# Kernel tuning notes

Measured on AMD Instinct MI355X. Metric: run time of the kernel, lower is better.

Reference implementation:

```python
import jax, jax.numpy as jnp
import numpy as np

N_Q = 16
N_K = 16
D_QK = 64
D_V = 64
# torch module default scale=1.0 saturates softmax at feature width 1024;
# we use the conventional sqrt(d) scale for well-conditioned numerics.
SCALE = 32.0  # sqrt(N_Q * D_QK)
DROPOUT_P = 0.0  # dropout is identity at p=0


def setup_inputs() -> dict:
    key = jax.random.key(0)
    kq, kk, kv = jax.random.split(key, 3)
    S = 8192
    return {
        "query": jax.random.normal(kq, (S, N_Q, D_QK), dtype=jnp.float32),
        "key": jax.random.normal(kk, (S, N_K, D_QK), dtype=jnp.float32),
        "value": jax.random.normal(kv, (S, N_K, D_V), dtype=jnp.float32),
    }


def reference(query, key, value):
    # Flatten trailing (head, dim) into one feature axis, as the torch view does.
    q = query.reshape(-1, N_Q * D_QK)            # [S_q, 1024]
    k = key.reshape(-1, N_K * D_QK)              # [S_k, 1024]
    v = value.reshape(-1, N_K * D_V)             # [S_k, 1024]
    scores = jnp.matmul(q, k.T) / SCALE          # [S_q, S_k]
    attn = jax.nn.softmax(scores, axis=-1)       # dropout_p=0 -> identity
    out = jnp.matmul(attn, v)                    # [S_q, 1024]
    return out.reshape(query.shape[:-1] + (-1,))  # [S_q, N_Q, D_V]
```

## Files before the change

### kernel.cpp

```cpp
#include <hip/hip_runtime.h>
#include <hip/hip_bf16.h>


typedef __bf16 bf16x8 __attribute__((ext_vector_type(8)));
typedef float f32x4 __attribute__((ext_vector_type(4)));
typedef const __attribute__((address_space(1))) unsigned int* as1p;
typedef __attribute__((address_space(3))) unsigned int* as3p;
typedef unsigned short u16;

__device__ __forceinline__ u16 f2bf(float x) {
  unsigned u = __float_as_uint(x);
  u += 0x7fffu + ((u >> 16) & 1u);
  return (u16)(u >> 16);
}
__device__ __forceinline__ float bf2f(u16 b) { return __uint_as_float(((unsigned)b) << 16); }
__device__ __forceinline__ unsigned pack2(float lo, float hi) {
  return (unsigned)f2bf(lo) | ((unsigned)f2bf(hi) << 16);
}

#define BAR()   do { __builtin_amdgcn_s_barrier(); __builtin_amdgcn_sched_barrier(0); } while (0)
#define LGKM0() do { asm volatile("s_waitcnt lgkmcnt(0)" ::: "memory"); __builtin_amdgcn_sched_barrier(0); } while (0)

__global__ __launch_bounds__(256) void cvt_bf16(const float* __restrict__ in,
                                                unsigned short* __restrict__ out) {
  const size_t i = (size_t)blockIdx.x * 256 + threadIdx.x;
  const float4* p = (const float4*)in + i * 2;
  float4 a = p[0], b = p[1];
  uint4 o;
  o.x = pack2(a.x, a.y);
  o.y = pack2(a.z, a.w);
  o.z = pack2(b.x, b.y);
  o.w = pack2(b.z, b.w);
  ((uint4*)out)[i] = o;
}

__global__ __launch_bounds__(256) void transpose_bf16(const float* __restrict__ V,
                                                      unsigned short* __restrict__ VT) {
  __shared__ float t[64][65];
  const int rb = blockIdx.x * 64;
  const int cb = blockIdx.y * 64;
  const int tid = threadIdx.x;
#pragma unroll
  for (int it = 0; it < 4; ++it) {
    int r = it * 16 + (tid >> 4);
    int c = (tid & 15) * 4;
    float4 x = *(const float4*)(V + (size_t)(rb + r) * 1024 + cb + c);
    t[r][c] = x.x; t[r][c + 1] = x.y; t[r][c + 2] = x.z; t[r][c + 3] = x.w;
  }
  __syncthreads();
  const int j = tid & 63;
  const int c0 = (tid >> 6) * 16;
#pragma unroll
  for (int i = 0; i < 16; ++i) {
    int c = c0 + i;
    VT[(size_t)(cb + c) * 8192 + rb + j] = f2bf(t[j][c]);
  }
}

template <int BM, int DEPTH, int OUTMODE>
__global__ __launch_bounds__(512, 2) void gemm_ring(const u16* __restrict__ A,
                                                    const u16* __restrict__ B,
                                                    void* __restrict__ Cv,
                                                    const float* __restrict__ inv,
                                                    float* __restrict__ partials,
                                                    int K, int ldc, int ntn, float scale) {
  constexpr int MF = BM / 32;
  constexpr int LA = BM / 64;
  constexpr int LB = 4;
  constexpr int ABUF = BM * 128;
  constexpr int BBUF = 256 * 128;
  constexpr int BUFSZ = ABUF + BBUF;
  constexpr int LPT = LA + LB;

  __shared__ __align__(1024) char smem[DEPTH * BUFSZ];

  const int tid = threadIdx.x;
  const int lane = tid & 63, wave = tid >> 6;
  const int wr = wave >> 2, wc = wave & 3;
  const int lan15 = lane & 15, g = lane >> 4, l7 = lane & 7;

  const int nwg = gridDim.x;
  const int wg = (blockIdx.x & 7) * (nwg >> 3) + (blockIdx.x >> 3);
  const int bm0 = (wg / ntn) * BM;
  const int bn0 = (wg % ntn) * 256;

  const int sr = tid >> 3;
  const int scb = ((tid & 7) ^ (sr & 7)) * 8;
  const u16* Ags = A + (size_t)(bm0 + sr) * K + scb;
  const u16* Bgs = B + (size_t)(bn0 + sr) * K + scb;

  const int sa0 = ((0 + g) ^ l7) * 16;
  const int sa1 = ((4 + g) ^ l7) * 16;
  const int abase = (wr * (BM / 2) + lan15) * 128;
  const int bbase = ABUF + (wc * 64 + lan15) * 128;

  f32x4 acc[MF][4];
#pragma unroll
  for (int m = 0; m < MF; ++m)
#pragma unroll
    for (int n = 0; n < 4; ++n) acc[m][n] = f32x4{0.f, 0.f, 0.f, 0.f};

  const int nt = K >> 6;

  auto ISSUE = [&](int t, int off) {
    const size_t ko = (size_t)t * 64;
#pragma unroll
    for (int j = 0; j < LA; ++j)
      __builtin_amdgcn_global_load_lds((as1p)(Ags + (size_t)j * 64 * K + ko),
                                       (as3p)(smem + off + j * 8192 + tid * 16), 16, 0, 0);
#pragma unroll
    for (int j = 0; j < LB; ++j)
      __builtin_amdgcn_global_load_lds((as1p)(Bgs + (size_t)j * 64 * K + ko),
                                       (as3p)(smem + off + ABUF + j * 8192 + tid * 16), 16, 0, 0);
  };

#pragma unroll
  for (int p = 0; p < DEPTH - 1; ++p)
    if (p < nt) ISSUE(p, p * BUFSZ);

  int cbuf = 0;
  int ibuf = (DEPTH - 1) * BUFSZ;
  if (ibuf >= DEPTH * BUFSZ) ibuf -= DEPTH * BUFSZ;

  bf16x8 af[4][2], bf[4][2];

  for (int t = 0; t < nt; ++t) {
    if (t + DEPTH - 2 < nt) {
      if constexpr (DEPTH == 3) asm volatile("s_waitcnt vmcnt(6)" ::: "memory");
      else                      asm volatile("s_waitcnt vmcnt(0)" ::: "memory");
    } else {
      asm volatile("s_waitcnt vmcnt(0)" ::: "memory");
    }
    __builtin_amdgcn_sched_barrier(0);
    BAR();

    if (t + DEPTH - 1 < nt) ISSUE(t + DEPTH - 1, ibuf);

    if constexpr (MF == 8) {
#pragma unroll
      for (int mh = 0; mh < 2; ++mh) {
#pragma unroll
        for (int m = 0; m < 4; ++m) {
          af[m][0] = *(const bf16x8*)(smem + cbuf + abase + (mh * 4 + m) * 2048 + sa0);
          af[m][1] = *(const bf16x8*)(smem + cbuf + abase + (mh * 4 + m) * 2048 + sa1);
        }
        if (mh == 0) {
#pragma unroll
          for (int n = 0; n < 4; ++n) {
            bf[n][0] = *(const bf16x8*)(smem + cbuf + bbase + n * 2048 + sa0);
            bf[n][1] = *(const bf16x8*)(smem + cbuf + bbase + n * 2048 + sa1);
          }
        }
        LGKM0();
        __builtin_amdgcn_s_setprio(1);
#pragma unroll
        for (int m = 0; m < 4; ++m)
#pragma unroll
          for (int n = 0; n < 4; ++n)
#pragma unroll
            for (int ks = 0; ks < 2; ++ks)
              acc[mh * 4 + m][n] =
                  __builtin_amdgcn_mfma_f32_16x16x32_bf16(af[m][ks], bf[n][ks], acc[mh * 4 + m][n], 0, 0, 0);
        __builtin_amdgcn_s_setprio(0);
      }
    } else {
#pragma unroll
      for (int ks = 0; ks < 2; ++ks) {
        const int sa = (ks == 0) ? sa0 : sa1;
#pragma unroll
        for (int m = 0; m < 4; ++m)
          af[m][ks] = *(const bf16x8*)(smem + cbuf + abase + m * 2048 + sa);
#pragma unroll
        for (int n = 0; n < 4; ++n)
          bf[n][ks] = *(const bf16x8*)(smem + cbuf + bbase + n * 2048 + sa);
        LGKM0();
        __builtin_amdgcn_s_setprio(1);
#pragma unroll
        for (int m = 0; m < 4; ++m)
#pragma unroll
          for (int n = 0; n < 4; ++n)
            acc[m][n] = __builtin_amdgcn_mfma_f32_16x16x32_bf16(af[m][ks], bf[n][ks], acc[m][n], 0, 0, 0);
        __builtin_amdgcn_s_setprio(0);
      }
    }

    cbuf += BUFSZ; if (cbuf == DEPTH * BUFSZ) cbuf = 0;
    ibuf += BUFSZ; if (ibuf == DEPTH * BUFSZ) ibuf = 0;
  }

  const int c0 = bn0 + wc * 64 + lan15;
  if constexpr (OUTMODE == 0) {
    u16* C = (u16*)Cv;
    const int cb4 = (bn0 >> 8) * 4 + wc;
#pragma unroll
    for (int m = 0; m < MF; ++m)
#pragma unroll
      for (int r = 0; r < 4; ++r) {
        const int row = bm0 + wr * (BM / 2) + m * 16 + g * 4 + r;
        float part = 0.f;
#pragma unroll
        for (int n = 0; n < 4; ++n) {
          float v = __expf(acc[m][n][r] * scale);
          C[(size_t)row * ldc + c0 + n * 16] = f2bf(v);
          part += v;
        }
        part += __shfl_xor(part, 1, 64);
        part += __shfl_xor(part, 2, 64);
        part += __shfl_xor(part, 4, 64);
        part += __shfl_xor(part, 8, 64);
        if (lan15 == 0) partials[(size_t)row * 128 + cb4] = part;
      }
  } else {
    float* C = (float*)Cv;
#pragma unroll
    for (int m = 0; m < MF; ++m)
#pragma unroll
      for (int r = 0; r < 4; ++r) {
        const int row = bm0 + wr * (BM / 2) + m * 16 + g * 4 + r;
        const float iv = inv ? inv[row] : 1.0f;
#pragma unroll
        for (int n = 0; n < 4; ++n)
          C[(size_t)row * ldc + c0 + n * 16] = acc[m][n][r] * iv;
      }
  }
}

__global__ __launch_bounds__(256) void rowinv(const float* __restrict__ partials,
                                              float* __restrict__ inv) {
  const int row = blockIdx.x * 256 + threadIdx.x;
  const float4* p = (const float4*)(partials + (size_t)row * 128);
  float s = 0.f;
#pragma unroll
  for (int j = 0; j < 32; ++j) {
    float4 v = p[j];
    s += (v.x + v.y) + (v.z + v.w);
  }
  inv[row] = 1.0f / s;
}

__global__ __launch_bounds__(256) void normalize_inplace(u16* __restrict__ E) {
  __shared__ float red[4];
  u16* row = E + (size_t)blockIdx.x * 8192;
  const int tid = threadIdx.x;
  float f[32];
  float s = 0.f;
#pragma unroll
  for (int c = 0; c < 4; ++c) {
    uint4 v = *((const uint4*)row + c * 256 + tid);
    unsigned u[4] = {v.x, v.y, v.z, v.w};
#pragma unroll
    for (int q = 0; q < 4; ++q) {
      f[c * 8 + q * 2] = bf2f((u16)(u[q] & 0xffffu));
      f[c * 8 + q * 2 + 1] = bf2f((u16)(u[q] >> 16));
      s += f[c * 8 + q * 2] + f[c * 8 + q * 2 + 1];
    }
  }
#pragma unroll
  for (int off = 32; off; off >>= 1) s += __shfl_xor(s, off, 64);
  if ((tid & 63) == 0) red[tid >> 6] = s;
  __syncthreads();
  const float iv = 1.0f / ((red[0] + red[1]) + (red[2] + red[3]));
#pragma unroll
  for (int c = 0; c < 4; ++c) {
    uint4 o;
    o.x = pack2(f[c * 8 + 0] * iv, f[c * 8 + 1] * iv);
    o.y = pack2(f[c * 8 + 2] * iv, f[c * 8 + 3] * iv);
    o.z = pack2(f[c * 8 + 4] * iv, f[c * 8 + 5] * iv);
    o.w = pack2(f[c * 8 + 6] * iv, f[c * 8 + 7] * iv);
    *((uint4*)row + c * 256 + tid) = o;
  }
}

extern "C" void kernel_launch(void* const* d_in, const int* in_sizes, int n_in,
                              void* d_out, int out_size, void* d_ws, size_t ws_size,
                              hipStream_t stream) {
  const float* Q = (const float*)d_in[0];
  const float* K = (const float*)d_in[1];
  const float* V = (const float*)d_in[2];

  char* ws = (char*)d_ws;
  u16* S = (u16*)ws;
  u16* VT = (u16*)(ws + (size_t)134217728);
  float* partials = (float*)(ws + (size_t)134217728 + 16777216);
  float* inv = (float*)(ws + (size_t)134217728 + 16777216 + 4194304);
  const bool haveInv =
      ws_size >= (size_t)134217728 + 16777216 + 4194304 + 32768;

  u16* Qb = (u16*)d_out;
  u16* Kb = Qb + 8388608;

  cvt_bf16<<<4096, 256, 0, stream>>>(Q, Qb);
  cvt_bf16<<<4096, 256, 0, stream>>>(K, Kb);
  transpose_bf16<<<dim3(128, 16), 256, 0, stream>>>(V, VT);

  gemm_ring<256, 2, 0><<<1024, 512, 0, stream>>>(
      Qb, Kb, S, nullptr, haveInv ? partials : (float*)(ws + 134217728 + 16777216),
      1024, 8192, 32, 1.0f / 32.0f);

  if (haveInv) {
    rowinv<<<32, 256, 0, stream>>>(partials, inv);
    gemm_ring<128, 3, 1><<<256, 512, 0, stream>>>(
        S, VT, d_out, inv, nullptr, 8192, 1024, 4, 1.0f);
  } else {
    normalize_inplace<<<8192, 256, 0, stream>>>(S);
    gemm_ring<128, 3, 1><<<256, 512, 0, stream>>>(
        S, VT, d_out, nullptr, nullptr, 8192, 1024, 4, 1.0f);
  }
}
```

Measured before the change: 313.1 us.

## Restructure GEMM mainloop into 8-phase interleaved load/MFMA schedule with double buffering

Replaces the ring-buffered GEMM loop with a two-buffer schedule. Each K-tile is split into four quadrant MFMA phases. Global-to-LDS loads are issued in small units between phases, and LDS fragment reads are interleaved with them, so memory traffic overlaps with matrix-core work at a finer grain. The PV GEMM drops from a 3-deep to a 2-deep buffer, freeing LDS. In exchange there are many more barriers per tile and a hand-tuned vmcnt accounting that must match the issue order.

```diff
diff --git a/kernel.cpp b/kernel.cpp
--- a/kernel.cpp
+++ b/kernel.cpp
@@ -20,6 +20,7 @@
 
 #define BAR()   do { __builtin_amdgcn_s_barrier(); __builtin_amdgcn_sched_barrier(0); } while (0)
 #define LGKM0() do { asm volatile("s_waitcnt lgkmcnt(0)" ::: "memory"); __builtin_amdgcn_sched_barrier(0); } while (0)
+#define VM(n)   do { asm volatile("s_waitcnt vmcnt(" #n ")" ::: "memory"); __builtin_amdgcn_sched_barrier(0); } while (0)
 
 __global__ __launch_bounds__(256) void cvt_bf16(const float* __restrict__ in,
                                                 unsigned short* __restrict__ out) {
@@ -57,22 +58,22 @@
   }
 }
 
-template <int BM, int DEPTH, int OUTMODE>
-__global__ __launch_bounds__(512, 2) void gemm_ring(const u16* __restrict__ A,
-                                                    const u16* __restrict__ B,
-                                                    void* __restrict__ Cv,
-                                                    const float* __restrict__ inv,
-                                                    float* __restrict__ partials,
-                                                    int K, int ldc, int ntn, float scale) {
+template <int BM, int OUTMODE>
+__global__ __launch_bounds__(512, 2) void gemm8(const u16* __restrict__ A,
+                                                const u16* __restrict__ B,
+                                                void* __restrict__ Cv,
+                                                const float* __restrict__ inv,
+                                                float* __restrict__ partials,
+                                                int K, int ldc, int ntn, float scale) {
   constexpr int MF = BM / 32;
+  constexpr int MH = MF / 2;
   constexpr int LA = BM / 64;
-  constexpr int LB = 4;
+  constexpr int NU = (LA + 4) / 2;
   constexpr int ABUF = BM * 128;
-  constexpr int BBUF = 256 * 128;
+  constexpr int BBUF = 32768;
   constexpr int BUFSZ = ABUF + BBUF;
-  constexpr int LPT = LA + LB;
-
-  __shared__ __align__(1024) char smem[DEPTH * BUFSZ];
+  static_assert(NU == 3 || NU == 4, "");
+  __shared__ __align__(1024) char smem[2 * BUFSZ];
 
   const int tid = threadIdx.x;
   const int lane = tid & 63, wave = tid >> 6;
@@ -101,91 +102,99 @@
     for (int n = 0; n < 4; ++n) acc[m][n] = f32x4{0.f, 0.f, 0.f, 0.f};
 
   const int nt = K >> 6;
-
-  auto ISSUE = [&](int t, int off) {
+  const int niter = nt >> 1;
+
+  auto ISSUE_UNIT = [&](int t, int u) {
+    const int bb = (t & 1) * BUFSZ;
     const size_t ko = (size_t)t * 64;
-#pragma unroll
-    for (int j = 0; j < LA; ++j)
-      __builtin_amdgcn_global_load_lds((as1p)(Ags + (size_t)j * 64 * K + ko),
-                                       (as3p)(smem + off + j * 8192 + tid * 16), 16, 0, 0);
-#pragma unroll
-    for (int j = 0; j < LB; ++j)
-      __builtin_amdgcn_global_load_lds((as1p)(Bgs + (size_t)j * 64 * K + ko),
-                                       (as3p)(smem + off + ABUF + j * 8192 + tid * 16), 16, 0, 0);
-  };
-
-#pragma unroll
-  for (int p = 0; p < DEPTH - 1; ++p)
-    if (p < nt) ISSUE(p, p * BUFSZ);
-
-  int cbuf = 0;
-  int ibuf = (DEPTH - 1) * BUFSZ;
-  if (ibuf >= DEPTH * BUFSZ) ibuf -= DEPTH * BUFSZ;
-
-  bf16x8 af[4][2], bf[4][2];
-
-  for (int t = 0; t < nt; ++t) {
-    if (t + DEPTH - 2 < nt) {
-      if constexpr (DEPTH == 3) asm volatile("s_waitcnt vmcnt(6)" ::: "memory");
-      else                      asm volatile("s_waitcnt vmcnt(0)" ::: "memory");
-    } else {
-      asm volatile("s_waitcnt vmcnt(0)" ::: "memory");
-    }
-    __builtin_amdgcn_sched_barrier(0);
-    BAR();
-
-    if (t + DEPTH - 1 < nt) ISSUE(t + DEPTH - 1, ibuf);
-
-    if constexpr (MF == 8) {
-#pragma unroll
-      for (int mh = 0; mh < 2; ++mh) {
-#pragma unroll
-        for (int m = 0; m < 4; ++m) {
-          af[m][0] = *(const bf16x8*)(smem + cbuf + abase + (mh * 4 + m) * 2048 + sa0);
-          af[m][1] = *(const bf16x8*)(smem + cbuf + abase + (mh * 4 + m) * 2048 + sa1);
-        }
-        if (mh == 0) {
-#pragma unroll
-          for (int n = 0; n < 4; ++n) {
-            bf[n][0] = *(const bf16x8*)(smem + cbuf + bbase + n * 2048 + sa0);
-            bf[n][1] = *(const bf16x8*)(smem + cbuf + bbase + n * 2048 + sa1);
-          }
-        }
-        LGKM0();
-        __builtin_amdgcn_s_setprio(1);
-#pragma unroll
-        for (int m = 0; m < 4; ++m)
-#pragma unroll
-          for (int n = 0; n < 4; ++n)
-#pragma unroll
-            for (int ks = 0; ks < 2; ++ks)
-              acc[mh * 4 + m][n] =
-                  __builtin_amdgcn_mfma_f32_16x16x32_bf16(af[m][ks], bf[n][ks], acc[mh * 4 + m][n], 0, 0, 0);
-        __builtin_amdgcn_s_setprio(0);
+    if (2 * u < LA) {
+#pragma unroll
+      for (int s = 0; s < 2; ++s) {
+        const int j = 2 * u + s;
+        __builtin_amdgcn_global_load_lds((as1p)(Ags + (size_t)j * 64 * K + ko),
+                                         (as3p)(smem + bb + j * 8192 + tid * 16), 16, 0, 0);
       }
     } else {
 #pragma unroll
-      for (int ks = 0; ks < 2; ++ks) {
-        const int sa = (ks == 0) ? sa0 : sa1;
-#pragma unroll
-        for (int m = 0; m < 4; ++m)
-          af[m][ks] = *(const bf16x8*)(smem + cbuf + abase + m * 2048 + sa);
-#pragma unroll
-        for (int n = 0; n < 4; ++n)
-          bf[n][ks] = *(const bf16x8*)(smem + cbuf + bbase + n * 2048 + sa);
-        LGKM0();
-        __builtin_amdgcn_s_setprio(1);
-#pragma unroll
-        for (int m = 0; m < 4; ++m)
-#pragma unroll
-          for (int n = 0; n < 4; ++n)
-            acc[m][n] = __builtin_amdgcn_mfma_f32_16x16x32_bf16(af[m][ks], bf[n][ks], acc[m][n], 0, 0, 0);
-        __builtin_amdgcn_s_setprio(0);
+      for (int s = 0; s < 2; ++s) {
+        const int j = 2 * u - LA + s;
+        __builtin_amdgcn_global_load_lds((as1p)(Bgs + (size_t)j * 64 * K + ko),
+                                         (as3p)(smem + bb + ABUF + j * 8192 + tid * 16), 16, 0, 0);
       }
     }
-
-    cbuf += BUFSZ; if (cbuf == DEPTH * BUFSZ) cbuf = 0;
-    ibuf += BUFSZ; if (ibuf == DEPTH * BUFSZ) ibuf = 0;
+  };
+
+  bf16x8 a[MH][2], b[4][2];
+  auto DS_A = [&](int bb, int mh) {
+#pragma unroll
+    for (int m = 0; m < MH; ++m) {
+      a[m][0] = *(const bf16x8*)(smem + bb + abase + (mh * MH + m) * 2048 + sa0);
+      a[m][1] = *(const bf16x8*)(smem + bb + abase + (mh * MH + m) * 2048 + sa1);
+    }
+  };
+  auto DS_B = [&](int bb, int nh) {
+#pragma unroll
+    for (int n = 0; n < 2; ++n) {
+      b[nh * 2 + n][0] = *(const bf16x8*)(smem + bb + bbase + (nh * 2 + n) * 2048 + sa0);
+      b[nh * 2 + n][1] = *(const bf16x8*)(smem + bb + bbase + (nh * 2 + n) * 2048 + sa1);
+    }
+  };
+  auto MMA = [&](int mh, int nh) {
+    __builtin_amdgcn_s_setprio(1);
+#pragma unroll
+    for (int m = 0; m < MH; ++m)
+#pragma unroll
+      for (int n = 0; n < 2; ++n)
+#pragma unroll
+        for (int ks = 0; ks < 2; ++ks)
+          acc[mh * MH + m][nh * 2 + n] = __builtin_amdgcn_mfma_f32_16x16x32_bf16(
+              a[m][ks], b[nh * 2 + n][ks], acc[mh * MH + m][nh * 2 + n], 0, 0, 0);
+    __builtin_amdgcn_s_setprio(0);
+  };
+
+#pragma unroll
+  for (int u = 0; u < NU; ++u) ISSUE_UNIT(0, u);
+  ISSUE_UNIT(1, 0);
+  VM(2);
+  BAR();
+
+  for (int i = 0; i < niter; ++i) {
+    const int t0 = 2 * i;
+    const bool more = (i + 1 < niter);
+
+    DS_A(0, 0); DS_B(0, 0);
+    ISSUE_UNIT(t0 + 1, 1);
+    BAR(); LGKM0(); MMA(0, 0); BAR();
+
+    DS_B(0, 1);
+    if constexpr (NU >= 3) ISSUE_UNIT(t0 + 1, 2);
+    BAR(); LGKM0(); MMA(0, 1); BAR();
+
+    DS_A(0, 1);
+    if constexpr (NU >= 4) ISSUE_UNIT(t0 + 1, 3);
+    BAR(); LGKM0(); MMA(1, 0); BAR();
+
+    if (more) ISSUE_UNIT(t0 + 2, 0);
+    BAR(); MMA(1, 1);
+    if (more) { VM(2); } else { VM(0); }
+    BAR();
+
+    DS_A(BUFSZ, 0); DS_B(BUFSZ, 0);
+    if (more) ISSUE_UNIT(t0 + 2, 1);
+    BAR(); LGKM0(); MMA(0, 0); BAR();
+
+    DS_B(BUFSZ, 1);
+    if (more) { if constexpr (NU >= 3) ISSUE_UNIT(t0 + 2, 2); }
+    BAR(); LGKM0(); MMA(0, 1); BAR();
+
+    DS_A(BUFSZ, 1);
+    if (more) { if constexpr (NU >= 4) ISSUE_UNIT(t0 + 2, 3); }
+    BAR(); LGKM0(); MMA(1, 0); BAR();
+
+    if (more) ISSUE_UNIT(t0 + 3, 0);
+    BAR(); MMA(1, 1);
+    if (more) { VM(2); } else { VM(0); }
+    BAR();
   }
 
   const int c0 = bn0 + wc * 64 + lan15;
@@ -293,17 +302,17 @@
   cvt_bf16<<<4096, 256, 0, stream>>>(K, Kb);
   transpose_bf16<<<dim3(128, 16), 256, 0, stream>>>(V, VT);
 
-  gemm_ring<256, 2, 0><<<1024, 512, 0, stream>>>(
+  gemm8<256, 0><<<1024, 512, 0, stream>>>(
       Qb, Kb, S, nullptr, haveInv ? partials : (float*)(ws + 134217728 + 16777216),
       1024, 8192, 32, 1.0f / 32.0f);
 
   if (haveInv) {
     rowinv<<<32, 256, 0, stream>>>(partials, inv);
-    gemm_ring<128, 3, 1><<<256, 512, 0, stream>>>(
+    gemm8<128, 1><<<256, 512, 0, stream>>>(
         S, VT, d_out, inv, nullptr, 8192, 1024, 4, 1.0f);
   } else {
     normalize_inplace<<<8192, 256, 0, stream>>>(S);
-    gemm_ring<128, 3, 1><<<256, 512, 0, stream>>>(
+    gemm8<128, 1><<<256, 512, 0, stream>>>(
         S, VT, d_out, nullptr, nullptr, 8192, 1024, 4, 1.0f);
   }
 }
```

Result: no change. 310.4 us (-0.9%).
